# Kernel tuning notes

Measured on AMD Instinct MI355X. Metric: run time of the kernel, lower is better.

## Reference

```python
import jax, jax.numpy as jnp
import numpy as np

B, K, D = 131072, 256, 16


def setup_inputs() -> dict:
    key = jax.random.key(0)
    k1, k2 = jax.random.split(key)
    trajectory = jax.random.normal(k1, (B, D), dtype=jnp.float32)
    centers = jax.random.normal(k2, (K, D), dtype=jnp.float32)
    return {"trajectory": trajectory, "centers": centers}


def reference(trajectory, centers):
    # dists[b, k] = ||centers[k] - trajectory[b]||_2 ; argmin over k.
    # Computed via the expanded squared distance to avoid materializing the
    # [B, K, D] broadcast difference tensor (same argmin as torch's norm).
    x2 = jnp.sum(trajectory * trajectory, axis=-1, keepdims=True)      # [B, 1]
    c2 = jnp.sum(centers * centers, axis=-1)                            # [K]
    xc = jnp.einsum('bd,kd->bk', trajectory, centers)                   # [B, K]
    d2 = x2 - 2.0 * xc + c2[None, :]                                    # [B, K]
    center_idxs = jnp.argmin(d2, axis=1)                                # [B]
    offset = trajectory - centers[center_idxs]                          # [B, D]
    return center_idxs, offset
```

## Files before the change

kernel.cpp:

```cpp
#include <hip/hip_runtime.h>


constexpr int Bn = 131072;
constexpr int Kn = 256;
constexpr int Dn = 16;
constexpr int PTS = 64;
constexpr int NW = 4;
constexpr int KC = Kn / NW;

__global__ __launch_bounds__(256, 8) void kmeans_kernel(
    const float* __restrict__ traj, const float* __restrict__ centers,
    float* __restrict__ out) {
  __shared__ float c2s[Kn];
  __shared__ float sbest[NW * PTS];
  __shared__ int sbi[NW * PTS];
  __shared__ int swin[PTS];

  const int t = threadIdx.x;
  const int blk = blockIdx.x;

  {
    const float4* cp = reinterpret_cast<const float4*>(centers + t * Dn);
    float4 a = cp[0], b = cp[1], c = cp[2], d = cp[3];
    float s = 0.0f;
    s = fmaf(a.x, a.x, s); s = fmaf(a.y, a.y, s);
    s = fmaf(a.z, a.z, s); s = fmaf(a.w, a.w, s);
    s = fmaf(b.x, b.x, s); s = fmaf(b.y, b.y, s);
    s = fmaf(b.z, b.z, s); s = fmaf(b.w, b.w, s);
    s = fmaf(c.x, c.x, s); s = fmaf(c.y, c.y, s);
    s = fmaf(c.z, c.z, s); s = fmaf(c.w, c.w, s);
    s = fmaf(d.x, d.x, s); s = fmaf(d.y, d.y, s);
    s = fmaf(d.z, d.z, s); s = fmaf(d.w, d.w, s);
    c2s[t] = s;
  }
  __syncthreads();

  const int w = __builtin_amdgcn_readfirstlane(t >> 6);
  const int l = t & 63;
  const int p = blk * PTS + l;

  float y[Dn];
  {
    const float4* xp = reinterpret_cast<const float4*>(traj + (size_t)p * Dn);
    float4 v0 = xp[0], v1 = xp[1], v2 = xp[2], v3 = xp[3];
    y[0] = -2.0f * v0.x; y[1] = -2.0f * v0.y; y[2] = -2.0f * v0.z; y[3] = -2.0f * v0.w;
    y[4] = -2.0f * v1.x; y[5] = -2.0f * v1.y; y[6] = -2.0f * v1.z; y[7] = -2.0f * v1.w;
    y[8] = -2.0f * v2.x; y[9] = -2.0f * v2.y; y[10] = -2.0f * v2.z; y[11] = -2.0f * v2.w;
    y[12] = -2.0f * v3.x; y[13] = -2.0f * v3.y; y[14] = -2.0f * v3.z; y[15] = -2.0f * v3.w;
  }

  float best = __builtin_inff();
  int bi = 0;
  const int k0 = w * KC;
#pragma unroll 4
  for (int kk = 0; kk < KC; ++kk) {
    const int k = k0 + kk;
    const float* cr = centers + k * Dn;
    float acc = c2s[k];
#pragma unroll
    for (int d = 0; d < Dn; ++d) acc = fmaf(y[d], cr[d], acc);
    if (acc < best) { best = acc; bi = k; }
  }
  sbest[w * PTS + l] = best;
  sbi[w * PTS + l] = bi;
  __syncthreads();

  if (t < PTS) {
    float b0 = sbest[t];
    int i0 = sbi[t];
#pragma unroll
    for (int ww = 1; ww < NW; ++ww) {
      float b1 = sbest[ww * PTS + t];
      int i1 = sbi[ww * PTS + t];
      if (b1 < b0) { b0 = b1; i0 = i1; }
    }
    swin[t] = i0;
    out[blk * PTS + t] = (float)i0;
  }
  __syncthreads();

  {
    const int pb = t >> 2, q = t & 3;
    const int pt = blk * PTS + pb;
    const int win = swin[pb];
    float4 xv = reinterpret_cast<const float4*>(traj + (size_t)pt * Dn)[q];
    float4 cv = reinterpret_cast<const float4*>(centers + (size_t)win * Dn)[q];
    float4 o = make_float4(xv.x - cv.x, xv.y - cv.y, xv.z - cv.z, xv.w - cv.w);
    reinterpret_cast<float4*>(out + Bn)[(size_t)pt * 4 + q] = o;
  }
}

extern "C" void kernel_launch(void* const* d_in, const int* in_sizes, int n_in,
                              void* d_out, int out_size, void* d_ws, size_t ws_size,
                              hipStream_t stream) {
  const float* traj = (const float*)d_in[0];
  const float* centers = (const float*)d_in[1];
  float* out = (float*)d_out;
  kmeans_kernel<<<Bn / PTS, 256, 0, stream>>>(traj, centers, out);
}
```

Baseline: 79.94 us.

## Process two points per thread with packed float2 FMAs over centers

Each thread now handles two trajectory points, held as two-wide vectors, so each center coefficient load is reused across both points. The inner product uses packed two-lane FMA operations (v_pk_fma_f32 on CDNA), which can halve the FMA instruction count per point. Blocks cover 128 points instead of 64, halving the grid and the per-block overhead of computing the center norms. In exchange, register pressure rises, grid parallelism drops, and the compare/select work per point is unchanged.

Result: faster. 74.21 us (-7.2%).

```diff
diff --git a/kernel.cpp b/kernel.cpp
--- a/kernel.cpp
+++ b/kernel.cpp
@@ -4,9 +4,11 @@
 constexpr int Bn = 131072;
 constexpr int Kn = 256;
 constexpr int Dn = 16;
-constexpr int PTS = 64;
+constexpr int PTS = 128;
 constexpr int NW = 4;
 constexpr int KC = Kn / NW;
+
+typedef float v2f __attribute__((ext_vector_type(2)));
 
 __global__ __launch_bounds__(256, 8) void kmeans_kernel(
     const float* __restrict__ traj, const float* __restrict__ centers,
@@ -37,32 +39,44 @@
 
   const int w = __builtin_amdgcn_readfirstlane(t >> 6);
   const int l = t & 63;
-  const int p = blk * PTS + l;
+  const int p0 = blk * PTS + l;
+  const int p1 = p0 + 64;
 
-  float y[Dn];
+  v2f y[Dn];
   {
-    const float4* xp = reinterpret_cast<const float4*>(traj + (size_t)p * Dn);
-    float4 v0 = xp[0], v1 = xp[1], v2 = xp[2], v3 = xp[3];
-    y[0] = -2.0f * v0.x; y[1] = -2.0f * v0.y; y[2] = -2.0f * v0.z; y[3] = -2.0f * v0.w;
-    y[4] = -2.0f * v1.x; y[5] = -2.0f * v1.y; y[6] = -2.0f * v1.z; y[7] = -2.0f * v1.w;
-    y[8] = -2.0f * v2.x; y[9] = -2.0f * v2.y; y[10] = -2.0f * v2.z; y[11] = -2.0f * v2.w;
-    y[12] = -2.0f * v3.x; y[13] = -2.0f * v3.y; y[14] = -2.0f * v3.z; y[15] = -2.0f * v3.w;
+    const float4* xa = reinterpret_cast<const float4*>(traj + (size_t)p0 * Dn);
+    const float4* xb = reinterpret_cast<const float4*>(traj + (size_t)p1 * Dn);
+#pragma unroll
+    for (int q = 0; q < 4; ++q) {
+      float4 a = xa[q], b = xb[q];
+      y[q * 4 + 0] = (v2f){-2.0f * a.x, -2.0f * b.x};
+      y[q * 4 + 1] = (v2f){-2.0f * a.y, -2.0f * b.y};
+      y[q * 4 + 2] = (v2f){-2.0f * a.z, -2.0f * b.z};
+      y[q * 4 + 3] = (v2f){-2.0f * a.w, -2.0f * b.w};
+    }
   }
 
-  float best = __builtin_inff();
-  int bi = 0;
+  float best0 = __builtin_inff(), best1 = __builtin_inff();
+  int bi0 = 0, bi1 = 0;
   const int k0 = w * KC;
 #pragma unroll 4
   for (int kk = 0; kk < KC; ++kk) {
     const int k = k0 + kk;
     const float* cr = centers + k * Dn;
-    float acc = c2s[k];
+    const float c2k = c2s[k];
+    v2f acc = (v2f){c2k, c2k};
 #pragma unroll
-    for (int d = 0; d < Dn; ++d) acc = fmaf(y[d], cr[d], acc);
-    if (acc < best) { best = acc; bi = k; }
+    for (int d = 0; d < Dn; ++d) {
+      const float c = cr[d];
+      acc = y[d] * (v2f){c, c} + acc;
+    }
+    if (acc.x < best0) { best0 = acc.x; bi0 = k; }
+    if (acc.y < best1) { best1 = acc.y; bi1 = k; }
   }
-  sbest[w * PTS + l] = best;
-  sbi[w * PTS + l] = bi;
+  sbest[w * PTS + l] = best0;
+  sbi[w * PTS + l] = bi0;
+  sbest[w * PTS + 64 + l] = best1;
+  sbi[w * PTS + 64 + l] = bi1;
   __syncthreads();
 
   if (t < PTS) {
@@ -79,8 +93,10 @@
   }
   __syncthreads();
 
-  {
-    const int pb = t >> 2, q = t & 3;
+#pragma unroll
+  for (int it = 0; it < 2; ++it) {
+    const int id = it * 256 + t;
+    const int pb = id >> 2, q = id & 3;
     const int pt = blk * PTS + pb;
     const int win = swin[pb];
     float4 xv = reinterpret_cast<const float4*>(traj + (size_t)pt * Dn)[q];
@@ -93,6 +109,7 @@
 extern "C" void kernel_launch(void* const* d_in, const int* in_sizes, int n_in,
                               void* d_out, int out_size, void* d_ws, size_t ws_size,
                               hipStream_t stream) {
+  (void)in_sizes; (void)n_in; (void)out_size; (void)d_ws; (void)ws_size;
   const float* traj = (const float*)d_in[0];
   const float* centers = (const float*)d_in[1];
   float* out = (float*)d_out;
```
